# Kernel optimization log

Hardware: AMD Instinct MI355X
Metric: run time of the kernel (lower is better)

The kernel has to match this reference:

```python
import jax, jax.numpy as jnp
import numpy as np

HIDDEN = 1024
NUM_HEADS = 16
HEAD_DIM = HIDDEN // NUM_HEADS


def setup_inputs() -> dict:
    key = jax.random.key(0)
    ks = jax.random.split(key, 11)
    s = 1.0 / np.sqrt(HIDDEN)
    x = jax.random.normal(ks[0], (4, 2048, HIDDEN), dtype=jnp.float32)
    Wq = jax.random.uniform(ks[1], (HIDDEN, HIDDEN), jnp.float32, -s, s)
    bq = jax.random.uniform(ks[2], (HIDDEN,), jnp.float32, -s, s)
    Wk = jax.random.uniform(ks[3], (HIDDEN, HIDDEN), jnp.float32, -s, s)
    bk = jax.random.uniform(ks[4], (HIDDEN,), jnp.float32, -s, s)
    Wv = jax.random.uniform(ks[5], (HIDDEN, HIDDEN), jnp.float32, -s, s)
    bv = jax.random.uniform(ks[6], (HIDDEN,), jnp.float32, -s, s)
    Wo = jax.random.uniform(ks[7], (HIDDEN, HIDDEN), jnp.float32, -s, s)
    bo = jax.random.uniform(ks[8], (HIDDEN,), jnp.float32, -s, s)
    ln_g = jnp.ones((HIDDEN,), jnp.float32)
    ln_b = jnp.zeros((HIDDEN,), jnp.float32)
    return {"x": x, "Wq": Wq, "bq": bq, "Wk": Wk, "bk": bk,
            "Wv": Wv, "bv": bv, "Wo": Wo, "bo": bo,
            "ln_g": ln_g, "ln_b": ln_b}


def _layer_norm(x, g, b, eps=1e-5):
    mu = jnp.mean(x, axis=-1, keepdims=True)
    var = jnp.var(x, axis=-1, keepdims=True)
    return (x - mu) * jax.lax.rsqrt(var + eps) * g + b


def reference(x, Wq, bq, Wk, bk, Wv, bv, Wo, bo, ln_g, ln_b):
    B, S, _ = x.shape
    residual = x
    h = _layer_norm(x, ln_g, ln_b)
    # projections (torch Linear: y = h @ W.T + b)
    q = (h @ Wq.T + bq).reshape(B, S, NUM_HEADS, HEAD_DIM).transpose(0, 2, 1, 3)
    k = (h @ Wk.T + bk).reshape(B, S, NUM_HEADS, HEAD_DIM).transpose(0, 2, 1, 3)
    v = (h @ Wv.T + bv).reshape(B, S, NUM_HEADS, HEAD_DIM).transpose(0, 2, 1, 3)
    scores = jnp.einsum('bhqd,bhkd->bhqk', q, k) / np.sqrt(HEAD_DIM).astype(np.float32)
    weights = jax.nn.softmax(scores, axis=-1)  # dropout = identity (eval mode)
    context = jnp.einsum('bhqk,bhkd->bhqd', weights, v)
    context = context.transpose(0, 2, 1, 3).reshape(B, S, HIDDEN)
    out = context @ Wo.T + bo
    return out + residual
```

## Files before the change

kernel.cpp:

```cpp
#include <hip/hip_runtime.h>

typedef unsigned short u16;
typedef unsigned int   u32;
using bf16x8 = __attribute__((ext_vector_type(8))) __bf16;
using f32x4  = __attribute__((ext_vector_type(4))) float;

__device__ __forceinline__ float b2f(u16 u){ union { float f; u32 i; } v; v.i = ((u32)u) << 16; return v.f; }
__device__ __forceinline__ u16 f2b(float f){
  union { float f; u32 i; } v; v.f = f;
  u32 r = v.i + 0x7FFFu + ((v.i >> 16) & 1u);
  return (u16)(r >> 16);
}
__device__ __forceinline__ u32 pk_bf16_trunc(float a, float b){
  return __builtin_amdgcn_perm(__float_as_uint(b), __float_as_uint(a), 0x07060302u);
}

__global__ __launch_bounds__(256) void cvt_w(const float* __restrict__ s0, const float* __restrict__ s1,
                                             const float* __restrict__ s2, const float* __restrict__ s3,
                                             u16* __restrict__ d){
  const float* srcs[4] = {s0, s1, s2, s3};
  const float* s = srcs[blockIdx.y];
  u16* dd = d + (size_t)blockIdx.y * (1024u * 1024u);
  const int i = (blockIdx.x * 256 + threadIdx.x) * 4;
  float4 v = *(const float4*)(s + i);
  uint2 o;
  o.x = (u32)f2b(v.x) | ((u32)f2b(v.y) << 16);
  o.y = (u32)f2b(v.z) | ((u32)f2b(v.w) << 16);
  *(uint2*)(dd + i) = o;
}

__global__ __launch_bounds__(256) void ln_kernel(const float* __restrict__ x, const float* __restrict__ g,
                                                 const float* __restrict__ be, u16* __restrict__ h){
  const int row = blockIdx.x, tid = threadIdx.x;
  const float* xr = x + (size_t)row * 1024u;
  float4 raw = *(const float4*)(xr + tid * 4);
  float s  = raw.x + raw.y + raw.z + raw.w;
  float sq = raw.x*raw.x + raw.y*raw.y + raw.z*raw.z + raw.w*raw.w;
  #pragma unroll
  for (int m = 1; m < 64; m <<= 1){ s += __shfl_xor(s, m); sq += __shfl_xor(sq, m); }
  __shared__ float ws[4], wq[4];
  if ((tid & 63) == 0){ ws[tid >> 6] = s; wq[tid >> 6] = sq; }
  __syncthreads();
  s  = ws[0] + ws[1] + ws[2] + ws[3];
  sq = wq[0] + wq[1] + wq[2] + wq[3];
  const float mu = s * (1.0f / 1024.0f);
  const float rstd = rsqrtf(sq * (1.0f / 1024.0f) - mu * mu + 1e-5f);
  float4 gg = *(const float4*)(g + tid * 4);
  float4 bb = *(const float4*)(be + tid * 4);
  float y0 = (raw.x - mu) * rstd * gg.x + bb.x;
  float y1 = (raw.y - mu) * rstd * gg.y + bb.y;
  float y2 = (raw.z - mu) * rstd * gg.z + bb.z;
  float y3 = (raw.w - mu) * rstd * gg.w + bb.w;
  uint2 outv;
  outv.x = (u32)f2b(y0) | ((u32)f2b(y1) << 16);
  outv.y = (u32)f2b(y2) | ((u32)f2b(y3) << 16);
  *(uint2*)(h + (size_t)row * 1024u + tid * 4) = outv;
}

__global__ __launch_bounds__(256) void gemm_qkv(const u16* __restrict__ A, const u16* __restrict__ Wcat,
                                                const float* __restrict__ bq, const float* __restrict__ bk,
                                                const float* __restrict__ bv,
                                                u16* __restrict__ qo, u16* __restrict__ ko, u16* __restrict__ vo){
  __shared__ u16 lA[128 * 32];
  __shared__ u16 lB[128 * 32];
  const int tid = threadIdx.x;
  const int lane = tid & 63, wv = tid >> 6, l15 = lane & 15, quad = lane >> 4;
  const int wr = wv >> 1, wc = wv & 1;
  const int row0 = blockIdx.x * 128, col0 = blockIdx.y * 128;
  const int K = 1024;
  f32x4 acc[4][4] = {};
  for (int kt = 0; kt < 32; ++kt){
    __syncthreads();
    #pragma unroll
    for (int jj = 0; jj < 2; ++jj){
      int idx = jj * 256 + tid;
      int r = idx >> 2, c = idx & 3;
      __builtin_amdgcn_global_load_lds(
        (const __attribute__((address_space(1))) void*)(A + (size_t)(row0 + r) * K + (kt * 32 + c * 8)),
        (__attribute__((address_space(3))) void*)(&lA[idx * 8]), 16, 0, 0);
      __builtin_amdgcn_global_load_lds(
        (const __attribute__((address_space(1))) void*)(Wcat + (size_t)(col0 + r) * K + (kt * 32 + c * 8)),
        (__attribute__((address_space(3))) void*)(&lB[idx * 8]), 16, 0, 0);
    }
    __syncthreads();
    bf16x8 af[4], bf[4];
    #pragma unroll
    for (int i = 0; i < 4; ++i) af[i] = *(const bf16x8*)&lA[(wr * 64 + i * 16 + l15) * 32 + quad * 8];
    #pragma unroll
    for (int j = 0; j < 4; ++j) bf[j] = *(const bf16x8*)&lB[(wc * 64 + j * 16 + l15) * 32 + quad * 8];
    #pragma unroll
    for (int i = 0; i < 4; ++i)
      #pragma unroll
      for (int j = 0; j < 4; ++j)
        acc[i][j] = __builtin_amdgcn_mfma_f32_16x16x32_bf16(af[i], bf[j], acc[i][j], 0, 0, 0);
  }
  const int sel = col0 >> 10;
  const float* bias = (sel == 0) ? bq : (sel == 1) ? bk : bv;
  u16* dst = (sel == 0) ? qo : (sel == 1) ? ko : vo;
  #pragma unroll
  for (int i = 0; i < 4; ++i){
    const int grow = row0 + wr * 64 + i * 16 + quad * 4;
    #pragma unroll
    for (int j = 0; j < 4; ++j){
      const int gcol = (col0 & 1023) + wc * 64 + j * 16 + l15;
      const float bb = bias[gcol];
      #pragma unroll
      for (int r = 0; r < 4; ++r){
        size_t off = (size_t)(grow + r) * 1024u + gcol;
        dst[off] = f2b(acc[i][j][r] + bb);
      }
    }
  }
}

__global__ __launch_bounds__(256) void gemm_out(const u16* __restrict__ A, const u16* __restrict__ W,
                                                const float* __restrict__ bias, const float* __restrict__ res,
                                                float* __restrict__ C, int M, int N, int K){
  __shared__ u16 lA[128 * 32];
  __shared__ u16 lB[128 * 32];
  const int tid = threadIdx.x;
  const int lane = tid & 63, wv = tid >> 6, l15 = lane & 15, quad = lane >> 4;
  const int wr = wv >> 1, wc = wv & 1;
  const int row0 = blockIdx.x * 128, col0 = blockIdx.y * 128;
  f32x4 acc[4][4] = {};
  const int nkt = K >> 5;
  for (int kt = 0; kt < nkt; ++kt){
    __syncthreads();
    #pragma unroll
    for (int jj = 0; jj < 2; ++jj){
      int idx = jj * 256 + tid;
      int r = idx >> 2, c = idx & 3;
      __builtin_amdgcn_global_load_lds(
        (const __attribute__((address_space(1))) void*)(A + (size_t)(row0 + r) * K + (kt * 32 + c * 8)),
        (__attribute__((address_space(3))) void*)(&lA[idx * 8]), 16, 0, 0);
      __builtin_amdgcn_global_load_lds(
        (const __attribute__((address_space(1))) void*)(W + (size_t)(col0 + r) * K + (kt * 32 + c * 8)),
        (__attribute__((address_space(3))) void*)(&lB[idx * 8]), 16, 0, 0);
    }
    __syncthreads();
    bf16x8 af[4], bf[4];
    #pragma unroll
    for (int i = 0; i < 4; ++i) af[i] = *(const bf16x8*)&lA[(wr * 64 + i * 16 + l15) * 32 + quad * 8];
    #pragma unroll
    for (int j = 0; j < 4; ++j) bf[j] = *(const bf16x8*)&lB[(wc * 64 + j * 16 + l15) * 32 + quad * 8];
    #pragma unroll
    for (int i = 0; i < 4; ++i)
      #pragma unroll
      for (int j = 0; j < 4; ++j)
        acc[i][j] = __builtin_amdgcn_mfma_f32_16x16x32_bf16(af[i], bf[j], acc[i][j], 0, 0, 0);
  }
  #pragma unroll
  for (int i = 0; i < 4; ++i){
    const int grow = row0 + wr * 64 + i * 16 + quad * 4;
    #pragma unroll
    for (int j = 0; j < 4; ++j){
      const int gcol = col0 + wc * 64 + j * 16 + l15;
      const float bb = bias[gcol];
      #pragma unroll
      for (int r = 0; r < 4; ++r){
        size_t off = (size_t)(grow + r) * N + gcol;
        C[off] = acc[i][j][r] + bb + res[off];
      }
    }
  }
}

__global__ __launch_bounds__(256) void transpose_v(const u16* __restrict__ V, u16* __restrict__ Vt){
  __shared__ u16 t[64 * 66];
  const int bh = blockIdx.x >> 5, st = blockIdx.x & 31;
  const int b = bh >> 4, hh = bh & 15;
  const u16* Vg = V + ((size_t)b * 2048u + st * 64u) * 1024u + hh * 64;
  u16* Og = Vt + (size_t)bh * 64u * 2048u + st * 64u;
  #pragma unroll
  for (int i = 0; i < 16; ++i){
    int idx = i * 256 + threadIdx.x;
    int s = idx >> 6, d = idx & 63;
    t[s * 66 + d] = Vg[(size_t)s * 1024u + d];
  }
  __syncthreads();
  #pragma unroll
  for (int i = 0; i < 16; ++i){
    int idx = i * 256 + threadIdx.x;
    int d = idx >> 6, s = idx & 63;
    Og[(size_t)d * 2048u + s] = t[s * 66 + d];
  }
}

#define AS 72
#define PS2 40
__global__ __launch_bounds__(256, 4) void attn_kernel(const u16* __restrict__ Q, const u16* __restrict__ K,
                                                      const u16* __restrict__ Vt, u16* __restrict__ O){
  __shared__ u16 kls[64 * AS];
  __shared__ u16 vls[64 * AS];
  __shared__ u16 pls[128 * PS2];
  const int tid = threadIdx.x;
  const int lane = tid & 63, wv = tid >> 6, l15 = lane & 15, quad = lane >> 4;
  const int bh = blockIdx.x & 63, qt = blockIdx.x >> 6;
  const int b = bh >> 4, hh = bh & 15;
  const int q0 = qt * 128;
  const u16* Qg = Q + ((size_t)b * 2048u) * 1024u + hh * 64;
  const u16* Kg = K + ((size_t)b * 2048u) * 1024u + hh * 64;
  const u16* Vg = Vt + (size_t)bh * 64u * 2048u;
  u16* Og = O + ((size_t)b * 2048u) * 1024u + hh * 64;

  const int sidx = tid, sr = sidx >> 3, sc = sidx & 7;
  const int sr2 = (256 + sidx) >> 3, sc2 = (256 + sidx) & 7;

  const float QSCALE = 0.125f * 1.44269504f;
  bf16x8 qf2[2][2];
  #pragma unroll
  for (int g = 0; g < 2; ++g)
    #pragma unroll
    for (int kk = 0; kk < 2; ++kk){
      qf2[g][kk] = *(const bf16x8*)(Qg + (size_t)(q0 + wv * 32 + g * 16 + l15) * 1024u + kk * 32 + quad * 8);
      #pragma unroll
      for (int e = 0; e < 8; ++e) qf2[g][kk][e] = (__bf16)((float)qf2[g][kk][e] * QSCALE);
    }

  bf16x8 ones_f;
  {
    const __bf16 onev = (__bf16)1.0f, zerov = (__bf16)0.0f;
    #pragma unroll
    for (int e = 0; e < 8; ++e) ones_f[e] = (l15 == 0) ? onev : zerov;
  }

  f32x4 o2[2][4] = {};
  f32x4 o_l[2] = {};
  const f32x4 zf = {0.f, 0.f, 0.f, 0.f};

  uint4 kr0, kr1, vr0, vr1;
  {
    kr0 = *(const uint4*)(Kg + (size_t)sr * 1024u + sc * 8);
    vr0 = *(const uint4*)(Vg + (size_t)sr * 2048u + sc * 8);
    kr1 = *(const uint4*)(Kg + (size_t)sr2 * 1024u + sc2 * 8);
    vr1 = *(const uint4*)(Vg + (size_t)sr2 * 2048u + sc2 * 8);
  }

  for (int kt = 0; kt < 32; ++kt){
    __syncthreads();
    *(uint4*)&kls[sr  * AS + sc  * 8] = kr0;
    *(uint4*)&vls[sr  * AS + sc  * 8] = vr0;
    *(uint4*)&kls[sr2 * AS + sc2 * 8] = kr1;
    *(uint4*)&vls[sr2 * AS + sc2 * 8] = vr1;
    __syncthreads();
    if (kt < 31){
      const int s0 = (kt + 1) * 64;
      kr0 = *(const uint4*)(Kg + (size_t)(s0 + sr) * 1024u + sc * 8);
      vr0 = *(const uint4*)(Vg + (size_t)sr * 2048u + s0 + sc * 8);
      kr1 = *(const uint4*)(Kg + (size_t)(s0 + sr2) * 1024u + sc2 * 8);
      vr1 = *(const uint4*)(Vg + (size_t)sr2 * 2048u + s0 + sc2 * 8);
    }

    f32x4 s2[2][4];
    #pragma unroll
    for (int j = 0; j < 4; ++j){
      bf16x8 kfr0 = *(const bf16x8*)&kls[(j * 16 + l15) * AS + quad * 8];
      bf16x8 kfr1 = *(const bf16x8*)&kls[(j * 16 + l15) * AS + 32 + quad * 8];
      #pragma unroll
      for (int g = 0; g < 2; ++g){
        f32x4 a = __builtin_amdgcn_mfma_f32_16x16x32_bf16(kfr0, qf2[g][0], zf, 0, 0, 0);
        s2[g][j] = __builtin_amdgcn_mfma_f32_16x16x32_bf16(kfr1, qf2[g][1], a, 0, 0, 0);
      }
    }

    #pragma unroll
    for (int g = 0; g < 2; ++g)
      #pragma unroll
      for (int j = 0; j < 4; ++j)
        #pragma unroll
        for (int r = 0; r < 4; ++r)
          s2[g][j][r] = exp2f(s2[g][j][r]);

    #pragma unroll
    for (int kk = 0; kk < 2; ++kk){
      bf16x8 afr[2];
      #pragma unroll
      for (int g = 0; g < 2; ++g){
        u16* pw = &pls[(size_t)(wv * 32 + g * 16) * PS2];
        const int j0 = kk * 2, j1 = kk * 2 + 1;
        uint2 pk0, pk1;
        pk0.x = pk_bf16_trunc(s2[g][j0][0], s2[g][j0][1]);
        pk0.y = pk_bf16_trunc(s2[g][j0][2], s2[g][j0][3]);
        pk1.x = pk_bf16_trunc(s2[g][j1][0], s2[g][j1][1]);
        pk1.y = pk_bf16_trunc(s2[g][j1][2], s2[g][j1][3]);
        *(uint2*)&pw[l15 * PS2 + quad * 4]      = pk0;
        *(uint2*)&pw[l15 * PS2 + 16 + quad * 4] = pk1;
        afr[g] = *(const bf16x8*)&pw[l15 * PS2 + quad * 8];
      }
      #pragma unroll
      for (int g = 0; g < 2; ++g)
        o_l[g] = __builtin_amdgcn_mfma_f32_16x16x32_bf16(afr[g], ones_f, o_l[g], 0, 0, 0);
      #pragma unroll
      for (int j2 = 0; j2 < 4; ++j2){
        bf16x8 bfr = *(const bf16x8*)&vls[(j2 * 16 + l15) * AS + kk * 32 + quad * 8];
        #pragma unroll
        for (int g = 0; g < 2; ++g)
          o2[g][j2] = __builtin_amdgcn_mfma_f32_16x16x32_bf16(afr[g], bfr, o2[g][j2], 0, 0, 0);
      }
    }
  }

  #pragma unroll
  for (int g = 0; g < 2; ++g){
    float lr[4];
    #pragma unroll
    for (int r = 0; r < 4; ++r) lr[r] = 1.0f / __shfl(o_l[g][r], quad * 16);
    #pragma unroll
    for (int j2 = 0; j2 < 4; ++j2){
      #pragma unroll
      for (int r = 0; r < 4; ++r){
        const int qrow = q0 + wv * 32 + g * 16 + quad * 4 + r;
        const int d = j2 * 16 + l15;
        Og[(size_t)qrow * 1024u + d] = f2b(o2[g][j2][r] * lr[r]);
      }
    }
  }
}

extern "C" void kernel_launch(void* const* d_in, const int* in_sizes, int n_in,
                              void* d_out, int out_size, void* d_ws, size_t ws_size,
                              hipStream_t stream){
  (void)in_sizes; (void)n_in; (void)out_size; (void)ws_size;
  const float* x   = (const float*)d_in[0];
  const float* Wq  = (const float*)d_in[1];
  const float* bq  = (const float*)d_in[2];
  const float* Wk  = (const float*)d_in[3];
  const float* bk  = (const float*)d_in[4];
  const float* Wv  = (const float*)d_in[5];
  const float* bv  = (const float*)d_in[6];
  const float* Wo  = (const float*)d_in[7];
  const float* bo  = (const float*)d_in[8];
  const float* lng = (const float*)d_in[9];
  const float* lnb = (const float*)d_in[10];
  float* out = (float*)d_out;

  const size_t TE = (size_t)8192 * 1024;
  u16* ws0 = (u16*)d_ws;
  u16* ws1 = ws0 + TE;
  u16* ws2 = ws1 + TE;
  u16* wsw = ws2 + TE;
  u16* wob = wsw + (size_t)3 * 1024 * 1024;
  u16* v   = (u16*)d_out;

  cvt_w<<<dim3(1024, 4), 256, 0, stream>>>(Wq, Wk, Wv, Wo, wsw);
  ln_kernel<<<dim3(8192), 256, 0, stream>>>(x, lng, lnb, ws0);
  gemm_qkv<<<dim3(64, 24), 256, 0, stream>>>(ws0, wsw, bq, bk, bv, ws1, ws2, v);
  transpose_v<<<dim3(2048), 256, 0, stream>>>(v, ws0);
  attn_kernel<<<dim3(1024), 256, 0, stream>>>(ws1, ws2, ws0, ws1);
  gemm_out<<<dim3(64, 8), 256, 0, stream>>>(ws1, wob, bo, x, out, 8192, 1024, 1024);
}
```

Before: 312.6 us.

## Double-buffer K/V tiles, swizzle LDS, and use permlane swaps for P fragments

Splits the attention kernel's K/V shared memory into two buffers, so the next tile is written while the current one is consumed. This needs one barrier per iteration instead of two, and global loads are prefetched two tiles ahead. Padded LDS rows are replaced by an XOR swizzle, and the P-matrix round trip through shared memory is replaced by permlane32/16 swaps in registers. exp2f becomes the hardware exp2 builtin. The costs are more LDS per block, which may hurt occupancy at 4 blocks per CU, and correctness depends on the permlane lane mapping matching the MFMA layout.

New measurement: 287.7 us. 1.09x faster.

```diff
diff --git a/kernel.cpp b/kernel.cpp
--- a/kernel.cpp
+++ b/kernel.cpp
@@ -4,6 +4,7 @@
 typedef unsigned int   u32;
 using bf16x8 = __attribute__((ext_vector_type(8))) __bf16;
 using f32x4  = __attribute__((ext_vector_type(4))) float;
+using u32x2  = __attribute__((ext_vector_type(2))) unsigned int;
 
 __device__ __forceinline__ float b2f(u16 u){ union { float f; u32 i; } v; v.i = ((u32)u) << 16; return v.f; }
 __device__ __forceinline__ u16 f2b(float f){
@@ -186,13 +187,10 @@
   }
 }
 
-#define AS 72
-#define PS2 40
 __global__ __launch_bounds__(256, 4) void attn_kernel(const u16* __restrict__ Q, const u16* __restrict__ K,
                                                       const u16* __restrict__ Vt, u16* __restrict__ O){
-  __shared__ u16 kls[64 * AS];
-  __shared__ u16 vls[64 * AS];
-  __shared__ u16 pls[128 * PS2];
+  __shared__ u16 kls[2][64 * 64];
+  __shared__ u16 vls[2][64 * 64];
   const int tid = threadIdx.x;
   const int lane = tid & 63, wv = tid >> 6, l15 = lane & 15, quad = lane >> 4;
   const int bh = blockIdx.x & 63, qt = blockIdx.x >> 6;
@@ -203,8 +201,9 @@
   const u16* Vg = Vt + (size_t)bh * 64u * 2048u;
   u16* Og = O + ((size_t)b * 2048u) * 1024u + hh * 64;
 
-  const int sidx = tid, sr = sidx >> 3, sc = sidx & 7;
-  const int sr2 = (256 + sidx) >> 3, sc2 = (256 + sidx) & 7;
+  const int sr = tid >> 3, sc = tid & 7, sr2 = sr + 32;
+  const int sx = (sc ^ (sr & 7)) * 8;
+  const int c0 = ((quad ^ (l15 & 7))) * 8;
 
   const float QSCALE = 0.125f * 1.44269504f;
   bf16x8 qf2[2][2];
@@ -229,33 +228,46 @@
   const f32x4 zf = {0.f, 0.f, 0.f, 0.f};
 
   uint4 kr0, kr1, vr0, vr1;
-  {
-    kr0 = *(const uint4*)(Kg + (size_t)sr * 1024u + sc * 8);
-    vr0 = *(const uint4*)(Vg + (size_t)sr * 2048u + sc * 8);
-    kr1 = *(const uint4*)(Kg + (size_t)sr2 * 1024u + sc2 * 8);
-    vr1 = *(const uint4*)(Vg + (size_t)sr2 * 2048u + sc2 * 8);
-  }
+  kr0 = *(const uint4*)(Kg + (size_t)sr  * 1024u + sc * 8);
+  vr0 = *(const uint4*)(Vg + (size_t)sr  * 2048u + sc * 8);
+  kr1 = *(const uint4*)(Kg + (size_t)sr2 * 1024u + sc * 8);
+  vr1 = *(const uint4*)(Vg + (size_t)sr2 * 2048u + sc * 8);
+  *(uint4*)&kls[0][sr  * 64 + sx] = kr0;
+  *(uint4*)&vls[0][sr  * 64 + sx] = vr0;
+  *(uint4*)&kls[0][sr2 * 64 + sx] = kr1;
+  *(uint4*)&vls[0][sr2 * 64 + sx] = vr1;
+  kr0 = *(const uint4*)(Kg + (size_t)(64 + sr)  * 1024u + sc * 8);
+  vr0 = *(const uint4*)(Vg + (size_t)sr  * 2048u + 64 + sc * 8);
+  kr1 = *(const uint4*)(Kg + (size_t)(64 + sr2) * 1024u + sc * 8);
+  vr1 = *(const uint4*)(Vg + (size_t)sr2 * 2048u + 64 + sc * 8);
+  __syncthreads();
 
   for (int kt = 0; kt < 32; ++kt){
-    __syncthreads();
-    *(uint4*)&kls[sr  * AS + sc  * 8] = kr0;
-    *(uint4*)&vls[sr  * AS + sc  * 8] = vr0;
-    *(uint4*)&kls[sr2 * AS + sc2 * 8] = kr1;
-    *(uint4*)&vls[sr2 * AS + sc2 * 8] = vr1;
-    __syncthreads();
+    const int cur = kt & 1;
+    const u16* kb = kls[cur];
+    const u16* vb = vls[cur];
     if (kt < 31){
-      const int s0 = (kt + 1) * 64;
-      kr0 = *(const uint4*)(Kg + (size_t)(s0 + sr) * 1024u + sc * 8);
-      vr0 = *(const uint4*)(Vg + (size_t)sr * 2048u + s0 + sc * 8);
-      kr1 = *(const uint4*)(Kg + (size_t)(s0 + sr2) * 1024u + sc2 * 8);
-      vr1 = *(const uint4*)(Vg + (size_t)sr2 * 2048u + s0 + sc2 * 8);
+      u16* kw = kls[cur ^ 1];
+      u16* vw = vls[cur ^ 1];
+      *(uint4*)&kw[sr  * 64 + sx] = kr0;
+      *(uint4*)&vw[sr  * 64 + sx] = vr0;
+      *(uint4*)&kw[sr2 * 64 + sx] = kr1;
+      *(uint4*)&vw[sr2 * 64 + sx] = vr1;
+    }
+    if (kt < 30){
+      const int s0 = (kt + 2) * 64;
+      kr0 = *(const uint4*)(Kg + (size_t)(s0 + sr)  * 1024u + sc * 8);
+      vr0 = *(const uint4*)(Vg + (size_t)sr  * 2048u + s0 + sc * 8);
+      kr1 = *(const uint4*)(Kg + (size_t)(s0 + sr2) * 1024u + sc * 8);
+      vr1 = *(const uint4*)(Vg + (size_t)sr2 * 2048u + s0 + sc * 8);
     }
 
     f32x4 s2[2][4];
     #pragma unroll
     for (int j = 0; j < 4; ++j){
-      bf16x8 kfr0 = *(const bf16x8*)&kls[(j * 16 + l15) * AS + quad * 8];
-      bf16x8 kfr1 = *(const bf16x8*)&kls[(j * 16 + l15) * AS + 32 + quad * 8];
+      const int rb = (j * 16 + l15) * 64;
+      bf16x8 kfr0 = *(const bf16x8*)&kb[rb + c0];
+      bf16x8 kfr1 = *(const bf16x8*)&kb[rb + (c0 ^ 32)];
       #pragma unroll
       for (int g = 0; g < 2; ++g){
         f32x4 a = __builtin_amdgcn_mfma_f32_16x16x32_bf16(kfr0, qf2[g][0], zf, 0, 0, 0);
@@ -269,35 +281,38 @@
       for (int j = 0; j < 4; ++j)
         #pragma unroll
         for (int r = 0; r < 4; ++r)
-          s2[g][j][r] = exp2f(s2[g][j][r]);
+          s2[g][j][r] = __builtin_amdgcn_exp2f(s2[g][j][r]);
 
     #pragma unroll
     for (int kk = 0; kk < 2; ++kk){
       bf16x8 afr[2];
       #pragma unroll
       for (int g = 0; g < 2; ++g){
-        u16* pw = &pls[(size_t)(wv * 32 + g * 16) * PS2];
-        const int j0 = kk * 2, j1 = kk * 2 + 1;
-        uint2 pk0, pk1;
-        pk0.x = pk_bf16_trunc(s2[g][j0][0], s2[g][j0][1]);
-        pk0.y = pk_bf16_trunc(s2[g][j0][2], s2[g][j0][3]);
-        pk1.x = pk_bf16_trunc(s2[g][j1][0], s2[g][j1][1]);
-        pk1.y = pk_bf16_trunc(s2[g][j1][2], s2[g][j1][3]);
-        *(uint2*)&pw[l15 * PS2 + quad * 4]      = pk0;
-        *(uint2*)&pw[l15 * PS2 + 16 + quad * 4] = pk1;
-        afr[g] = *(const bf16x8*)&pw[l15 * PS2 + quad * 8];
+        const int j0 = kk * 2, j1 = j0 + 1;
+        u32 A0 = pk_bf16_trunc(s2[g][j0][0], s2[g][j0][1]);
+        u32 A1 = pk_bf16_trunc(s2[g][j0][2], s2[g][j0][3]);
+        u32 B0 = pk_bf16_trunc(s2[g][j1][0], s2[g][j1][1]);
+        u32 B1 = pk_bf16_trunc(s2[g][j1][2], s2[g][j1][3]);
+        u32x2 r1 = __builtin_amdgcn_permlane32_swap(A0, B0, false, false);
+        u32x2 r2 = __builtin_amdgcn_permlane16_swap(r1[0], r1[1], false, false);
+        u32x2 r3 = __builtin_amdgcn_permlane32_swap(A1, B1, false, false);
+        u32x2 r4 = __builtin_amdgcn_permlane16_swap(r3[0], r3[1], false, false);
+        union { uint4 u; bf16x8 v; } cv;
+        cv.u.x = r2[0]; cv.u.y = r4[0]; cv.u.z = r2[1]; cv.u.w = r4[1];
+        afr[g] = cv.v;
       }
       #pragma unroll
       for (int g = 0; g < 2; ++g)
         o_l[g] = __builtin_amdgcn_mfma_f32_16x16x32_bf16(afr[g], ones_f, o_l[g], 0, 0, 0);
       #pragma unroll
       for (int j2 = 0; j2 < 4; ++j2){
-        bf16x8 bfr = *(const bf16x8*)&vls[(j2 * 16 + l15) * AS + kk * 32 + quad * 8];
+        bf16x8 bfr = *(const bf16x8*)&vb[(j2 * 16 + l15) * 64 + (c0 ^ (kk * 32))];
         #pragma unroll
         for (int g = 0; g < 2; ++g)
           o2[g][j2] = __builtin_amdgcn_mfma_f32_16x16x32_bf16(afr[g], bfr, o2[g][j2], 0, 0, 0);
       }
     }
+    __syncthreads();
   }
 
   #pragma unroll
```
